# Optimization experiments

Measured on AMD Instinct MI355X. Metric: run time of the kernel, lower is better.

The kernel has to match this reference:

```python
import jax, jax.numpy as jnp
import numpy as np

H_SIZE = 128
E_SIZE = 16
N_LAYERS = 3
N_ATOMS = 80000
N_BLOCKS = 16000
N_EDGES = 320000
N_GRAPHS = 128


def setup_inputs() -> dict:
    key = jax.random.key(0)
    ks = jax.random.split(key, 20)
    p = lambda k, shape: (0.02 * jax.random.normal(k, shape, dtype=jnp.float32))
    h = H_SIZE
    inp = {
        'H': jax.random.normal(ks[0], (N_ATOMS, h), dtype=jnp.float32),
        'Z': jax.random.normal(ks[1], (N_ATOMS, 1, 3), dtype=jnp.float32),
        'block_id': jnp.sort(jax.random.randint(ks[2], (N_ATOMS,), 0, N_BLOCKS)),
        'batch_id': jnp.sort(jax.random.randint(ks[3], (N_BLOCKS,), 0, N_GRAPHS)),
        'edges': jax.random.randint(ks[4], (2, N_EDGES), 0, N_BLOCKS),
        'edge_attr': jax.random.normal(ks[5], (N_EDGES, E_SIZE), dtype=jnp.float32),
        # EGNN parameters
        'emb_in_w': p(ks[6], (h, h)), 'emb_in_b': jnp.zeros((h,), jnp.float32),
        'emb_out_w': p(ks[7], (h, h)), 'emb_out_b': jnp.zeros((h,), jnp.float32),
        'edge_w1': p(ks[8], (N_LAYERS, 2 * h + 1 + E_SIZE, h)), 'edge_b1': jnp.zeros((N_LAYERS, h), jnp.float32),
        'edge_w2': p(ks[9], (N_LAYERS, h, h)), 'edge_b2': jnp.zeros((N_LAYERS, h), jnp.float32),
        'node_w1': p(ks[10], (N_LAYERS, 2 * h, h)), 'node_b1': jnp.zeros((N_LAYERS, h), jnp.float32),
        'node_w2': p(ks[11], (N_LAYERS, h, h)), 'node_b2': jnp.zeros((N_LAYERS, h), jnp.float32),
        'coord_w1': p(ks[12], (N_LAYERS, h, h)), 'coord_b1': jnp.zeros((N_LAYERS, h), jnp.float32),
        'coord_w3': p(ks[13], (N_LAYERS, h, 1)),  # final coord layer, no bias
    }
    return inp


def _normalize(x, eps=1e-12):
    # F.normalize(dim=-1): x / max(||x||_2, eps)
    n = jnp.linalg.norm(x, axis=-1, keepdims=True)
    return x / jnp.maximum(n, eps)


def _seg_mean(x, ids, n):
    s = jax.ops.segment_sum(x, ids, num_segments=n)
    c = jax.ops.segment_sum(jnp.ones((x.shape[0], 1), x.dtype), ids, num_segments=n)
    return s / jnp.maximum(c, 1.0)


def _egnn_forward(H, Z, block_id, batch_id, edges, edge_attr,
                  emb_in_w, emb_in_b, emb_out_w, emb_out_b,
                  edge_w1, edge_b1, edge_w2, edge_b2,
                  node_w1, node_b1, node_w2, node_b2,
                  coord_w1, coord_b1, coord_w3):
    silu = jax.nn.silu
    # atom -> block pooling (scatter_mean)
    Hm = _seg_mean(H, block_id, N_BLOCKS)                      # [B, h]
    x = _seg_mean(Z.reshape(Z.shape[0], -1), block_id, N_BLOCKS)  # [B, 3] (squeeze of [B,1,3])
    row, col = edges[0], edges[1]

    h = Hm @ emb_in_w + emb_in_b
    for l in range(N_LAYERS):
        diff = x[row] - x[col]                                 # [E, 3]
        radial = jnp.sum(diff * diff, axis=-1, keepdims=True)  # [E, 1]
        e_in = jnp.concatenate([h[row], h[col], radial, edge_attr], axis=-1)  # [E, 2h+1+e]
        m = silu(silu(e_in @ edge_w1[l] + edge_b1[l]) @ edge_w2[l] + edge_b2[l])  # edge MLP [E, h]
        # coordinate update: per-edge scalar weight, mean aggregation
        w = silu(m @ coord_w1[l] + coord_b1[l]) @ coord_w3[l]  # [E, 1]
        x = x + _seg_mean(diff * w, row, N_BLOCKS)
        # node update: sum aggregation of messages, residual
        agg = jax.ops.segment_sum(m, row, num_segments=N_BLOCKS)  # [B, h]
        h = h + (silu(jnp.concatenate([h, agg], axis=-1) @ node_w1[l] + node_b1[l]) @ node_w2[l] + node_b2[l])
    h = h @ emb_out_w + emb_out_b

    block_repr = _normalize(h)                                  # [B, h]
    graph_repr = _normalize(jax.ops.segment_sum(block_repr, batch_id, num_segments=N_GRAPHS))  # [G, h]
    return Hm, block_repr, graph_repr


def reference(H, Z, block_id, batch_id, edges, edge_attr,
              emb_in_w, emb_in_b, emb_out_w, emb_out_b,
              edge_w1, edge_b1, edge_w2, edge_b2,
              node_w1, node_b1, node_w2, node_b2,
              coord_w1, coord_b1, coord_w3):
    return _egnn_forward(H, Z, block_id, batch_id, edges, edge_attr,
                         emb_in_w, emb_in_b, emb_out_w, emb_out_b,
                         edge_w1, edge_b1, edge_w2, edge_b2,
                         node_w1, node_b1, node_w2, node_b2,
                         coord_w1, coord_b1, coord_w3)
```

## Files before the change

### kernel.cpp

```cpp
#include <hip/hip_runtime.h>

#define N_ATOMS  80000
#define N_BLOCKS 16000
#define N_EDGES  320000
#define N_GRAPHS 128
#define HS       128

typedef unsigned short ushortT;
typedef __attribute__((ext_vector_type(8))) __bf16 bf16x8;
typedef __attribute__((ext_vector_type(8))) unsigned short ushort8;
typedef __attribute__((ext_vector_type(4))) float f32x4;

__device__ __forceinline__ unsigned short f2bf(float f){
  unsigned int u = __builtin_bit_cast(unsigned int, f);
  u = (u + 0x7FFFu + ((u >> 16) & 1u)) >> 16;
  return (unsigned short)u;
}
__device__ __forceinline__ ushortT f2bff(float f){
  __bf16 b = (__bf16)f;
  return __builtin_bit_cast(ushortT, b);
}
__device__ __forceinline__ float bf2f(ushortT u){
  unsigned int v = ((unsigned int)u) << 16;
  return __builtin_bit_cast(float, v);
}
__device__ __forceinline__ bf16x8 load8bf(const ushortT* p){
  uint4 u = *reinterpret_cast<const uint4*>(p);
  return __builtin_bit_cast(bf16x8, u);
}
__device__ __forceinline__ bf16x8 load8f_bf(const float* p){
  float4 a = *reinterpret_cast<const float4*>(p);
  float4 b = *reinterpret_cast<const float4*>(p + 4);
  ushort8 u = { f2bff(a.x), f2bff(a.y), f2bff(a.z), f2bff(a.w),
                f2bff(b.x), f2bff(b.y), f2bff(b.z), f2bff(b.w) };
  return __builtin_bit_cast(bf16x8, u);
}
__device__ __forceinline__ float silu(float v){
  return v * __builtin_amdgcn_rcpf(1.f + __expf(-v));
}

__device__ __forceinline__ int c_of_p(int p){
  int ks = p >> 5, lg = (p >> 3) & 3, j = p & 7;
  return 16 * (ks * 2 + (j >> 2)) + lg * 4 + (j & 3);
}

struct PrepParams {
  const float* ew1; const float* ew2; const float* cw1;
  const float* nw1; const float* nw2; const float* ei; const float* eo;
  const float* eb1;
  ushortT* W1atp; ushortT* W1btp; ushortT* W1ct; ushortT* W2tp; ushortT* CW1tp;
  ushortT* NW1t; ushortT* NW2t; ushortT* Eint; ushortT* Eoutt;
  float* b1p; int* hist;
};

__device__ __forceinline__ void tcvt(int idx, const float* __restrict__ src,
                                     ushortT* __restrict__ dst,
                                     int srcK, int row_off, int K, int N, int Kpad,
                                     int pn, int pk){
  int k = idx % Kpad;
  int rem = idx / Kpad;
  int n = rem % N;
  int l = rem / N;
  float v = 0.f;
  if (k < K){
    int kk = pk ? c_of_p(k) : k;
    int nn = pn ? c_of_p(n) : n;
    v = src[((size_t)l * srcK + row_off + kk) * N + nn];
  }
  dst[idx] = f2bf(v);
}

#define PREP_TOTAL (49152*5 + 12288 + 98304 + 16384*2 + 16000 + 384)

__global__ void prep_kernel(PrepParams P){
  int idx = blockIdx.x * 256 + threadIdx.x;
  if (idx < 49152){ tcvt(idx, P.ew1, P.W1atp, 273,   0, 128, 128, 128, 1, 0); return; }
  idx -= 49152;
  if (idx < 49152){ tcvt(idx, P.ew1, P.W1btp, 273, 128, 128, 128, 128, 1, 0); return; }
  idx -= 49152;
  if (idx < 12288){ tcvt(idx, P.ew1, P.W1ct,  273, 256,  17, 128,  32, 0, 0); return; }
  idx -= 12288;
  if (idx < 49152){ tcvt(idx, P.ew2, P.W2tp,  128,   0, 128, 128, 128, 0, 1); return; }
  idx -= 49152;
  if (idx < 49152){ tcvt(idx, P.cw1, P.CW1tp, 128,   0, 128, 128, 128, 0, 1); return; }
  idx -= 49152;
  if (idx < 98304){ tcvt(idx, P.nw1, P.NW1t,  256,   0, 256, 128, 256, 0, 0); return; }
  idx -= 98304;
  if (idx < 49152){ tcvt(idx, P.nw2, P.NW2t,  128,   0, 128, 128, 128, 0, 0); return; }
  idx -= 49152;
  if (idx < 16384){ tcvt(idx, P.ei,  P.Eint,  128,   0, 128, 128, 128, 0, 0); return; }
  idx -= 16384;
  if (idx < 16384){ tcvt(idx, P.eo,  P.Eoutt, 128,   0, 128, 128, 128, 0, 0); return; }
  idx -= 16384;
  if (idx < 16000){ P.hist[idx] = 0; return; }
  idx -= 16000;
  if (idx < 384){ int l = idx >> 7, p = idx & 127; P.b1p[idx] = P.eb1[l * 128 + c_of_p(p)]; }
}

__global__ void hist_bstart_kernel(const int* __restrict__ edges, int* __restrict__ hist,
                                   const int* __restrict__ bid, int* __restrict__ bstart){
  int b = blockIdx.x;
  if (b < N_EDGES / 256){
    int e = b * 256 + threadIdx.x;
    atomicAdd(&hist[edges[e]], 1);
  } else {
    int i = (b - N_EDGES / 256) * 256 + threadIdx.x;
    if (i <= N_BLOCKS){
      int lo = 0, hi = N_ATOMS;
      while (lo < hi){ int mid = (lo + hi) >> 1; if (bid[mid] < i) lo = mid + 1; else hi = mid; }
      bstart[i] = lo;
    }
  }
}

__global__ void scan_kernel(const int* __restrict__ hist, int* __restrict__ estart,
                            int* __restrict__ ecur){
  __shared__ int ps[256];
  int t = threadIdx.x;
  const int chunk = (N_BLOCKS + 255) / 256;
  int lo = t * chunk, hi = lo + chunk;
  if (hi > N_BLOCKS) hi = N_BLOCKS;
  int s = 0;
  for (int i = lo; i < hi; i++) s += hist[i];
  ps[t] = s;
  __syncthreads();
  for (int off = 1; off < 256; off <<= 1){
    int v = (t >= off) ? ps[t - off] : 0;
    __syncthreads();
    ps[t] += v;
    __syncthreads();
  }
  int base = (t == 0) ? 0 : ps[t - 1];
  for (int i = lo; i < hi; i++){ estart[i] = base; ecur[i] = base; base += hist[i]; }
  if (t == 255) estart[N_BLOCKS] = base;
}

__global__ void scatter_kernel(const int* __restrict__ edges, const float* __restrict__ attr,
                               int* __restrict__ ecur,
                               int* __restrict__ srow, int* __restrict__ scol,
                               ushortT* __restrict__ sattr){
  int e = blockIdx.x * 256 + threadIdx.x;
  if (e >= N_EDGES) return;
  int r = edges[e], c = edges[N_EDGES + e];
  int p = atomicAdd(&ecur[r], 1);
  srow[p] = r; scol[p] = c;
  ushortT buf[32];
  buf[0] = 0;
#pragma unroll
  for (int k = 0; k < 16; k++) buf[k + 1] = f2bf(attr[(size_t)e * 16 + k]);
#pragma unroll
  for (int k = 17; k < 32; k++) buf[k] = 0;
#pragma unroll
  for (int k = 0; k < 16; k++)
    reinterpret_cast<uint*>(sattr + (size_t)p * 32)[k] = reinterpret_cast<uint*>(buf)[k];
}

__global__ void pool_kernel(const float* __restrict__ H, const float* __restrict__ Z,
                            const int* __restrict__ start,
                            float* __restrict__ Hm, float* __restrict__ x,
                            float* __restrict__ gsum){
  int b = blockIdx.x;
  int t = threadIdx.x;
  if (b < 128) gsum[b * 128 + t] = 0.f;
  int s = start[b], e = start[b + 1];
  float inv = 1.f / (float)((e - s) > 0 ? (e - s) : 1);
  float sum = 0.f;
  for (int a = s; a < e; a++) sum += H[(size_t)a * HS + t];
  Hm[(size_t)b * HS + t] = sum * inv;
  if (t < 3){
    float sz = 0.f;
    for (int a = s; a < e; a++) sz += Z[a * 3 + t];
    x[b * 3 + t] = sz * inv;
  }
}

__global__ __launch_bounds__(256) void gemm_pq_kernel(
    const float* __restrict__ A,
    const ushortT* __restrict__ Wt, const float* __restrict__ bias,
    float* __restrict__ Cf,
    const ushortT* __restrict__ Wa, const ushortT* __restrict__ Wb,
    const float* __restrict__ b1p,
    ushortT* __restrict__ Pbf, ushortT* __restrict__ Qbf,
    float* __restrict__ agg, float* __restrict__ xacc){
  __shared__ __align__(16) ushortT t1_s[4][2048];
  int t = threadIdx.x; int lane = t & 63; int wv = t >> 6;
  int l15 = lane & 15, lg = lane >> 4;
  int base = blockIdx.x * 64 + wv * 16;
  int row = base + l15;
  {
    float4 z4 = {0.f, 0.f, 0.f, 0.f};
    float4* aggp = reinterpret_cast<float4*>(agg + (size_t)blockIdx.x * 64 * HS);
#pragma unroll
    for (int i = 0; i < 8; i++) aggp[t + 256 * i] = z4;
    if (t < 192) xacc[blockIdx.x * 192 + t] = 0.f;
  }
  ushortT* T1 = t1_s[wv];
  f32x4 zero = {0.f, 0.f, 0.f, 0.f};
  f32x4 acc[8];
#pragma unroll
  for (int n = 0; n < 8; n++) acc[n] = zero;
#pragma unroll
  for (int ks = 0; ks < 4; ks++){
    int k0 = ks * 32 + lg * 8;
    bf16x8 af = load8f_bf(A + (size_t)row * HS + k0);
#pragma unroll
    for (int n = 0; n < 8; n++){
      bf16x8 bf = load8bf(Wt + (size_t)(16 * n + l15) * HS + k0);
      acc[n] = __builtin_amdgcn_mfma_f32_16x16x32_bf16(af, bf, acc[n], 0, 0, 0);
    }
  }
#pragma unroll
  for (int n = 0; n < 8; n++){
    int col = 16 * n + l15;
    float bv = bias[col];
#pragma unroll
    for (int r = 0; r < 4; r++){
      int ro = base + lg * 4 + r;
      int er = lg * 4 + r;
      float hv = acc[n][r] + bv;
      Cf[(size_t)ro * HS + col] = hv;
      T1[(er * 128 + col) ^ ((er & 7) << 3)] = f2bff(hv);
    }
  }
  f32x4 accp[8], accq[8];
#pragma unroll
  for (int n = 0; n < 8; n++){ accp[n] = zero; accq[n] = zero; }
#pragma unroll
  for (int ks = 0; ks < 4; ks++){
    int k0 = ks * 32 + lg * 8;
    bf16x8 af = load8bf(&T1[(l15 * 128 + k0) ^ ((l15 & 7) << 3)]);
#pragma unroll
    for (int n = 0; n < 8; n++){
      accp[n] = __builtin_amdgcn_mfma_f32_16x16x32_bf16(af, load8bf(Wa + (size_t)(16 * n + l15) * HS + k0), accp[n], 0, 0, 0);
      accq[n] = __builtin_amdgcn_mfma_f32_16x16x32_bf16(af, load8bf(Wb + (size_t)(16 * n + l15) * HS + k0), accq[n], 0, 0, 0);
    }
  }
#pragma unroll
  for (int n = 0; n < 8; n++){
    int col = 16 * n + l15;
    float bv = b1p[col];
#pragma unroll
    for (int r = 0; r < 4; r++){
      int ro = base + lg * 4 + r;
      Pbf[(size_t)ro * HS + col] = f2bff(accp[n][r] + bv);
      Qbf[(size_t)ro * HS + col] = f2bff(accq[n][r]);
    }
  }
}

template<bool PQ>
__global__ __launch_bounds__(256) void node_kernel(
    float* __restrict__ h, float* __restrict__ agg,
    const ushortT* __restrict__ W1t, const ushortT* __restrict__ W2t,
    const float* __restrict__ b1, const float* __restrict__ b2,
    const ushortT* __restrict__ Wa, const ushortT* __restrict__ Wb,
    const float* __restrict__ b1p,
    ushortT* __restrict__ Pbf, ushortT* __restrict__ Qbf,
    float* __restrict__ x, float* __restrict__ xacc, const int* __restrict__ estart){
  __shared__ __align__(16) ushortT t1_s[4][2048];
  int t = threadIdx.x; int lane = t & 63; int wv = t >> 6;
  int l15 = lane & 15, lg = lane >> 4;
  int base = blockIdx.x * 64 + wv * 16;
  int row = base + l15;
  ushortT* T1 = t1_s[wv];
  f32x4 zero = {0.f, 0.f, 0.f, 0.f};

  if (PQ){
    if (t < 192){
      int i = blockIdx.x * 192 + t;
      int b = i / 3;
      int cnt = estart[b + 1] - estart[b];
      x[i] += xacc[i] / (float)(cnt > 0 ? cnt : 1);
      xacc[i] = 0.f;
    }
  }

  f32x4 acc[8];
#pragma unroll
  for (int n = 0; n < 8; n++) acc[n] = zero;
#pragma unroll
  for (int ks = 0; ks < 8; ks++){
    int k0 = ks * 32 + lg * 8;
    bf16x8 af = (k0 < 128) ? load8f_bf(h + (size_t)row * HS + k0)
                           : load8f_bf(agg + (size_t)row * HS + (k0 - 128));
#pragma unroll
    for (int n = 0; n < 8; n++){
      acc[n] = __builtin_amdgcn_mfma_f32_16x16x32_bf16(af, load8bf(W1t + (size_t)(16 * n + l15) * 256 + k0), acc[n], 0, 0, 0);
    }
  }
  if (PQ){
    __syncthreads();
    float4 z4 = {0.f, 0.f, 0.f, 0.f};
    float4* aggp = reinterpret_cast<float4*>(agg + (size_t)blockIdx.x * 64 * HS);
#pragma unroll
    for (int i = 0; i < 8; i++) aggp[t + 256 * i] = z4;
  }
#pragma unroll
  for (int n = 0; n < 8; n++){
    int col = 16 * n + l15;
    float bv = b1[col];
#pragma unroll
    for (int r = 0; r < 4; r++){
      int er = lg * 4 + r;
      T1[(er * 128 + col) ^ ((er & 7) << 3)] = f2bff(silu(acc[n][r] + bv));
    }
  }
#pragma unroll
  for (int n = 0; n < 8; n++) acc[n] = zero;
#pragma unroll
  for (int ks = 0; ks < 4; ks++){
    int k0 = ks * 32 + lg * 8;
    bf16x8 af = load8bf(&T1[(l15 * 128 + k0) ^ ((l15 & 7) << 3)]);
#pragma unroll
    for (int n = 0; n < 8; n++){
      acc[n] = __builtin_amdgcn_mfma_f32_16x16x32_bf16(af, load8bf(W2t + (size_t)(16 * n + l15) * HS + k0), acc[n], 0, 0, 0);
    }
  }
#pragma unroll
  for (int n = 0; n < 8; n++){
    int col = 16 * n + l15;
    float bv = b2[col];
#pragma unroll
    for (int r = 0; r < 4; r++){
      int ro = base + lg * 4 + r;
      int er = lg * 4 + r;
      float hv = h[(size_t)ro * HS + col] + acc[n][r] + bv;
      h[(size_t)ro * HS + col] = hv;
      if (PQ) T1[(er * 128 + col) ^ ((er & 7) << 3)] = f2bff(hv);
    }
  }
  if (PQ){
    f32x4 accp[8], accq[8];
#pragma unroll
    for (int n = 0; n < 8; n++){ accp[n] = zero; accq[n] = zero; }
#pragma unroll
    for (int ks = 0; ks < 4; ks++){
      int k0 = ks * 32 + lg * 8;
      bf16x8 af = load8bf(&T1[(l15 * 128 + k0) ^ ((l15 & 7) << 3)]);
#pragma unroll
      for (int n = 0; n < 8; n++){
        accp[n] = __builtin_amdgcn_mfma_f32_16x16x32_bf16(af, load8bf(Wa + (size_t)(16 * n + l15) * HS + k0), accp[n], 0, 0, 0);
        accq[n] = __builtin_amdgcn_mfma_f32_16x16x32_bf16(af, load8bf(Wb + (size_t)(16 * n + l15) * HS + k0), accq[n], 0, 0, 0);
      }
    }
#pragma unroll
    for (int n = 0; n < 8; n++){
      int col = 16 * n + l15;
      float bv = b1p[col];
#pragma unroll
      for (int r = 0; r < 4; r++){
        int ro = base + lg * 4 + r;
        Pbf[(size_t)ro * HS + col] = f2bff(accp[n][r] + bv);
        Qbf[(size_t)ro * HS + col] = f2bff(accq[n][r]);
      }
    }
  }
}

__global__ __launch_bounds__(256) void emb_norm_kernel(
    const float* __restrict__ h, const ushortT* __restrict__ Wt,
    const float* __restrict__ bias, const int* __restrict__ batch_id,
    float* __restrict__ brep, float* __restrict__ gsum){
  int t = threadIdx.x; int lane = t & 63; int wv = t >> 6;
  int l15 = lane & 15, lg = lane >> 4;
  int base = blockIdx.x * 64 + wv * 16;
  int row = base + l15;
  f32x4 zero = {0.f, 0.f, 0.f, 0.f};
  f32x4 acc[8];
#pragma unroll
  for (int n = 0; n < 8; n++) acc[n] = zero;
#pragma unroll
  for (int ks = 0; ks < 4; ks++){
    int k0 = ks * 32 + lg * 8;
    bf16x8 af = load8f_bf(h + (size_t)row * HS + k0);
#pragma unroll
    for (int n = 0; n < 8; n++){
      acc[n] = __builtin_amdgcn_mfma_f32_16x16x32_bf16(af, load8bf(Wt + (size_t)(16 * n + l15) * HS + k0), acc[n], 0, 0, 0);
    }
  }
#pragma unroll
  for (int n = 0; n < 8; n++){
    float bv = bias[16 * n + l15];
#pragma unroll
    for (int r = 0; r < 4; r++) acc[n][r] += bv;
  }
  float scl[4];
#pragma unroll
  for (int r = 0; r < 4; r++){
    float ss = 0.f;
#pragma unroll
    for (int n = 0; n < 8; n++) ss += acc[n][r] * acc[n][r];
#pragma unroll
    for (int o = 1; o < 16; o <<= 1) ss += __shfl_xor(ss, o, 64);
    scl[r] = 1.f / fmaxf(sqrtf(ss), 1e-12f);
  }
#pragma unroll
  for (int r = 0; r < 4; r++){
    int ro = base + lg * 4 + r;
    int g = batch_id[ro];
#pragma unroll
    for (int n = 0; n < 8; n++){
      int col = 16 * n + l15;
      float v = acc[n][r] * scl[r];
      brep[(size_t)ro * HS + col] = v;
      atomicAdd(&gsum[g * HS + col], v);
    }
  }
}

template<int COORD>
__global__ __launch_bounds__(256, 4) void edge_kernel(
    const int* __restrict__ srow, const int* __restrict__ scol,
    const ushortT* __restrict__ sattr,
    const float* __restrict__ x,
    const ushortT* __restrict__ Pbf, const ushortT* __restrict__ Qbf,
    const ushortT* __restrict__ W1ct, const ushortT* __restrict__ W2tp,
    const ushortT* __restrict__ CW1tp,
    const float* __restrict__ b2, const float* __restrict__ cb1,
    const float* __restrict__ cw3,
    float* __restrict__ xacc, float* __restrict__ agg){
  __shared__ float bias_l[3][128];
  __shared__ int   rid_s[64];
  __shared__ float dif_s[COORD ? 64 : 1][3];
  __shared__ float wall[COORD ? 4 : 1][COORD ? 64 : 1];
  __shared__ __align__(16) ushortT S1[64 * 128];
  __shared__ __align__(16) ushortT S2[64 * 128];

  const int t = threadIdx.x;
  const int lane = t & 63;
  const int wv = t >> 6;
  const int l15 = lane & 15, lg = lane >> 4;
  const f32x4 zero = {0.f, 0.f, 0.f, 0.f};

  if (t < 128){
    bias_l[0][t] = b2[t];
    if (COORD){ bias_l[1][t] = cb1[t]; bias_l[2][t] = cw3[t]; }
  }

  const int erow = wv * 16 + l15;
  const int e = blockIdx.x * 64 + erow;
  const int r = srow[e], c = scol[e];
  const float dx = x[r * 3 + 0] - x[c * 3 + 0];
  const float dy = x[r * 3 + 1] - x[c * 3 + 1];
  const float dz = x[r * 3 + 2] - x[c * 3 + 2];
  const float rad = dx * dx + dy * dy + dz * dz;
  if (lg == 0){
    rid_s[erow] = r;
    if (COORD){ dif_s[erow][0] = dx; dif_s[erow][1] = dy; dif_s[erow][2] = dz; }
  }
  ushort8 at8 = __builtin_bit_cast(ushort8, load8bf(sattr + (size_t)e * 32 + lg * 8));
  if (lg == 0) at8[0] = f2bff(rad);
  const bf16x8 atb = __builtin_bit_cast(bf16x8, at8);

#pragma unroll
  for (int ks = 0; ks < 4; ks++){
    f32x4 a0 = __builtin_amdgcn_mfma_f32_16x16x32_bf16(
        load8bf(W1ct + (size_t)(16 * (2 * ks)     + l15) * 32 + lg * 8), atb, zero, 0, 0, 0);
    f32x4 a1 = __builtin_amdgcn_mfma_f32_16x16x32_bf16(
        load8bf(W1ct + (size_t)(16 * (2 * ks + 1) + l15) * 32 + lg * 8), atb, zero, 0, 0, 0);
    ushort8 pv = __builtin_bit_cast(ushort8, load8bf(Pbf + (size_t)r * HS + ks * 32 + lg * 8));
    ushort8 qv = __builtin_bit_cast(ushort8, load8bf(Qbf + (size_t)c * HS + ks * 32 + lg * 8));
    ushort8 af;
#pragma unroll
    for (int j = 0; j < 4; j++)
      af[j] = f2bff(silu(a0[j] + bf2f(pv[j]) + bf2f(qv[j])));
#pragma unroll
    for (int j = 4; j < 8; j++)
      af[j] = f2bff(silu(a1[j - 4] + bf2f(pv[j]) + bf2f(qv[j])));
    int byte = (erow * 256 + ks * 64 + lg * 16) ^ ((erow & 7) << 4);
    *reinterpret_cast<uint4*>(reinterpret_cast<char*>(S1) + byte) = __builtin_bit_cast(uint4, af);
  }
  __syncthreads();

  f32x4 acc2[4][2];
#pragma unroll
  for (int et = 0; et < 4; et++){ acc2[et][0] = zero; acc2[et][1] = zero; }
#pragma unroll
  for (int ks = 0; ks < 4; ks++){
    bf16x8 wf0 = load8bf(W2tp + (size_t)(16 * (2 * wv)     + l15) * HS + ks * 32 + lg * 8);
    bf16x8 wf1 = load8bf(W2tp + (size_t)(16 * (2 * wv + 1) + l15) * HS + ks * 32 + lg * 8);
#pragma unroll
    for (int et = 0; et < 4; et++){
      int row2 = et * 16 + l15;
      int byte = (row2 * 256 + ks * 64 + lg * 16) ^ ((row2 & 7) << 4);
      bf16x8 mb = __builtin_bit_cast(bf16x8,
          *reinterpret_cast<const uint4*>(reinterpret_cast<const char*>(S1) + byte));
      acc2[et][0] = __builtin_amdgcn_mfma_f32_16x16x32_bf16(wf0, mb, acc2[et][0], 0, 0, 0);
      acc2[et][1] = __builtin_amdgcn_mfma_f32_16x16x32_bf16(wf1, mb, acc2[et][1], 0, 0, 0);
    }
  }
#pragma unroll
  for (int g = 0; g < 2; g++){
    int n = 2 * wv + g;
    float4 bv = *reinterpret_cast<const float4*>(&bias_l[0][16 * n + lg * 4]);
    int pbyte = ((n >> 1) * 32 + lg * 8 + (n & 1) * 4) * 2;
#pragma unroll
    for (int et = 0; et < 4; et++){
      ushortT mm[4];
#pragma unroll
      for (int rr = 0; rr < 4; rr++)
        mm[rr] = f2bff(silu(acc2[et][g][rr] + (&bv.x)[rr]));
      int row2 = et * 16 + l15;
      int byte = (row2 * 256 + pbyte) ^ ((row2 & 7) << 4);
      *reinterpret_cast<uint2*>(reinterpret_cast<char*>(S2) + byte) =
          *reinterpret_cast<uint2*>(mm);
    }
  }
  __syncthreads();

  if (COORD){
    f32x4 acc3[4][2];
#pragma unroll
    for (int et = 0; et < 4; et++){ acc3[et][0] = zero; acc3[et][1] = zero; }
#pragma unroll
    for (int ks = 0; ks < 4; ks++){
      bf16x8 wf0 = load8bf(CW1tp + (size_t)(16 * (2 * wv)     + l15) * HS + ks * 32 + lg * 8);
      bf16x8 wf1 = load8bf(CW1tp + (size_t)(16 * (2 * wv + 1) + l15) * HS + ks * 32 + lg * 8);
#pragma unroll
      for (int et = 0; et < 4; et++){
        int row2 = et * 16 + l15;
        int byte = (row2 * 256 + ks * 64 + lg * 16) ^ ((row2 & 7) << 4);
        bf16x8 mb = __builtin_bit_cast(bf16x8,
            *reinterpret_cast<const uint4*>(reinterpret_cast<const char*>(S2) + byte));
        acc3[et][0] = __builtin_amdgcn_mfma_f32_16x16x32_bf16(wf0, mb, acc3[et][0], 0, 0, 0);
        acc3[et][1] = __builtin_amdgcn_mfma_f32_16x16x32_bf16(wf1, mb, acc3[et][1], 0, 0, 0);
      }
    }
#pragma unroll
    for (int et = 0; et < 4; et++){
      float ws = 0.f;
#pragma unroll
      for (int g = 0; g < 2; g++){
        int n = 2 * wv + g;
        float4 cbv = *reinterpret_cast<const float4*>(&bias_l[1][16 * n + lg * 4]);
        float4 cwv = *reinterpret_cast<const float4*>(&bias_l[2][16 * n + lg * 4]);
#pragma unroll
        for (int rr = 0; rr < 4; rr++)
          ws += silu(acc3[et][g][rr] + (&cbv.x)[rr]) * (&cwv.x)[rr];
      }
      ws += __shfl_xor(ws, 16, 64);
      ws += __shfl_xor(ws, 32, 64);
      if (lg == 0) wall[wv][et * 16 + l15] = ws;
    }
  }

  {
    const int c0 = c_of_p(2 * lane), c1 = c_of_p(2 * lane + 1);
    float run0 = 0.f, run1 = 0.f;
    int prev = __builtin_amdgcn_readfirstlane(rid_s[wv * 16]);
#pragma unroll
    for (int e2 = 0; e2 < 16; e2++){
      int re = __builtin_amdgcn_readfirstlane(rid_s[wv * 16 + e2]);
      if (re != prev){
        atomicAdd(&agg[(size_t)prev * HS + c0], run0);
        atomicAdd(&agg[(size_t)prev * HS + c1], run1);
        run0 = 0.f; run1 = 0.f; prev = re;
      }
      int row2 = wv * 16 + e2;
      int byte = (row2 * 256 + lane * 4) ^ ((row2 & 7) << 4);
      uint u = *reinterpret_cast<const uint*>(reinterpret_cast<const char*>(S2) + byte);
      run0 += bf2f((ushortT)(u & 0xFFFF));
      run1 += bf2f((ushortT)(u >> 16));
    }
    atomicAdd(&agg[(size_t)prev * HS + c0], run0);
    atomicAdd(&agg[(size_t)prev * HS + c1], run1);
  }

  if (COORD){
    __syncthreads();
    if (t < 192){
      int e2 = t / 3, cd = t % 3;
      float w = wall[0][e2] + wall[1][e2] + wall[2][e2] + wall[3][e2];
      atomicAdd(&xacc[(size_t)rid_s[e2] * 3 + cd], dif_s[e2][cd] * w);
    }
  }
}

__global__ void norm_graph_kernel(const float* __restrict__ gsum, float* __restrict__ grep){
  int wv = threadIdx.x >> 6, lane = threadIdx.x & 63;
  int g = blockIdx.x * 4 + wv;
  if (g >= N_GRAPHS) return;
  float v0 = gsum[g * HS + lane];
  float v1 = gsum[g * HS + 64 + lane];
  float ss = v0 * v0 + v1 * v1;
#pragma unroll
  for (int o = 1; o < 64; o <<= 1) ss += __shfl_xor(ss, o, 64);
  float s = 1.f / fmaxf(sqrtf(ss), 1e-12f);
  grep[(size_t)g * HS + lane] = v0 * s;
  grep[(size_t)g * HS + 64 + lane] = v1 * s;
}

extern "C" void kernel_launch(void* const* d_in, const int* in_sizes, int n_in,
                              void* d_out, int out_size, void* d_ws, size_t ws_size,
                              hipStream_t stream){
  const float* H         = (const float*)d_in[0];
  const float* Z         = (const float*)d_in[1];
  const int*   block_id  = (const int*)d_in[2];
  const int*   batch_id  = (const int*)d_in[3];
  const int*   edges     = (const int*)d_in[4];
  const float* edge_attr = (const float*)d_in[5];
  const float* emb_in_w  = (const float*)d_in[6];
  const float* emb_in_b  = (const float*)d_in[7];
  const float* emb_out_w = (const float*)d_in[8];
  const float* emb_out_b = (const float*)d_in[9];
  const float* edge_w1   = (const float*)d_in[10];
  const float* edge_b1   = (const float*)d_in[11];
  const float* edge_w2   = (const float*)d_in[12];
  const float* edge_b2   = (const float*)d_in[13];
  const float* node_w1   = (const float*)d_in[14];
  const float* node_b1   = (const float*)d_in[15];
  const float* node_w2   = (const float*)d_in[16];
  const float* node_b2   = (const float*)d_in[17];
  const float* coord_w1  = (const float*)d_in[18];
  const float* coord_b1  = (const float*)d_in[19];
  const float* coord_w3  = (const float*)d_in[20];

  float* out  = (float*)d_out;
  float* Hm   = out;
  float* brep = out + (size_t)N_BLOCKS * HS;
  float* grep = out + (size_t)2 * N_BLOCKS * HS;

  char* base = (char*)d_ws;
  size_t off = 0;
  auto take = [&](size_t bytes) -> char* {
    char* p = base + off;
    off += (bytes + 255) & ~(size_t)255;
    return p;
  };
  float*   x     = (float*)  take((size_t)N_BLOCKS * 3 * 4);
  float*   xacc  = (float*)  take((size_t)N_BLOCKS * 3 * 4);
  float*   h     = (float*)  take((size_t)N_BLOCKS * HS * 4);
  float*   agg   = (float*)  take((size_t)N_BLOCKS * HS * 4);
  float*   gsum  = (float*)  take((size_t)N_GRAPHS * HS * 4);
  int*     bstart= (int*)    take((size_t)(N_BLOCKS + 1) * 4);
  int*     hist  = (int*)    take((size_t)N_BLOCKS * 4);
  int*     estart= (int*)    take((size_t)(N_BLOCKS + 1) * 4);
  int*     ecur  = (int*)    take((size_t)N_BLOCKS * 4);
  int*     srow  = (int*)    take((size_t)N_EDGES * 4);
  int*     scol  = (int*)    take((size_t)N_EDGES * 4);
  ushortT* sattr = (ushortT*)take((size_t)N_EDGES * 32 * 2);
  ushortT* Pbf   = (ushortT*)take((size_t)N_BLOCKS * HS * 2);
  ushortT* Qbf   = (ushortT*)take((size_t)N_BLOCKS * HS * 2);
  ushortT* W1atp = (ushortT*)take((size_t)3 * 128 * 128 * 2);
  ushortT* W1btp = (ushortT*)take((size_t)3 * 128 * 128 * 2);
  ushortT* W1ct  = (ushortT*)take((size_t)3 * 128 * 32 * 2);
  ushortT* W2tp  = (ushortT*)take((size_t)3 * 128 * 128 * 2);
  ushortT* CW1tp = (ushortT*)take((size_t)3 * 128 * 128 * 2);
  ushortT* NW1t  = (ushortT*)take((size_t)3 * 128 * 256 * 2);
  ushortT* NW2t  = (ushortT*)take((size_t)3 * 128 * 128 * 2);
  ushortT* Eint  = (ushortT*)take((size_t)128 * 128 * 2);
  ushortT* Eoutt = (ushortT*)take((size_t)128 * 128 * 2);
  float*   b1p   = (float*)  take((size_t)3 * 128 * 4);

  PrepParams P;
  P.ew1 = edge_w1; P.ew2 = edge_w2; P.cw1 = coord_w1;
  P.nw1 = node_w1; P.nw2 = node_w2; P.ei = emb_in_w; P.eo = emb_out_w;
  P.eb1 = edge_b1;
  P.W1atp = W1atp; P.W1btp = W1btp; P.W1ct = W1ct; P.W2tp = W2tp; P.CW1tp = CW1tp;
  P.NW1t = NW1t; P.NW2t = NW2t; P.Eint = Eint; P.Eoutt = Eoutt;
  P.b1p = b1p; P.hist = hist;
  prep_kernel<<<(PREP_TOTAL + 255) / 256, 256, 0, stream>>>(P);

  hist_bstart_kernel<<<N_EDGES / 256 + (N_BLOCKS + 1 + 255) / 256, 256, 0, stream>>>(
      edges, hist, block_id, bstart);
  scan_kernel<<<1, 256, 0, stream>>>(hist, estart, ecur);
  scatter_kernel<<<N_EDGES / 256, 256, 0, stream>>>(edges, edge_attr, ecur, srow, scol, sattr);
  pool_kernel<<<N_BLOCKS, 128, 0, stream>>>(H, Z, bstart, Hm, x, gsum);

  gemm_pq_kernel<<<N_BLOCKS / 64, 256, 0, stream>>>(Hm, Eint, emb_in_b, h,
                                                    W1atp, W1btp, b1p, Pbf, Qbf, agg, xacc);

  for (int l = 0; l < 3; l++){
    if (l < 2){
      edge_kernel<1><<<N_EDGES / 64, 256, 0, stream>>>(
          srow, scol, sattr, x, Pbf, Qbf,
          W1ct + (size_t)l * 128 * 32, W2tp + (size_t)l * 128 * 128, CW1tp + (size_t)l * 128 * 128,
          edge_b2 + l * 128, coord_b1 + l * 128, coord_w3 + l * 128,
          xacc, agg);
      node_kernel<true><<<N_BLOCKS / 64, 256, 0, stream>>>(
          h, agg, NW1t + (size_t)l * 128 * 256, NW2t + (size_t)l * 128 * 128,
          node_b1 + l * 128, node_b2 + l * 128,
          W1atp + (size_t)(l + 1) * 128 * 128, W1btp + (size_t)(l + 1) * 128 * 128,
          b1p + (l + 1) * 128, Pbf, Qbf, x, xacc, estart);
    } else {
      edge_kernel<0><<<N_EDGES / 64, 256, 0, stream>>>(
          srow, scol, sattr, x, Pbf, Qbf,
          W1ct + (size_t)l * 128 * 32, W2tp + (size_t)l * 128 * 128, CW1tp + (size_t)l * 128 * 128,
          edge_b2 + l * 128, coord_b1 + l * 128, coord_w3 + l * 128,
          xacc, agg);
      node_kernel<false><<<N_BLOCKS / 64, 256, 0, stream>>>(
          h, agg, NW1t + (size_t)l * 128 * 256, NW2t + (size_t)l * 128 * 128,
          node_b1 + l * 128, node_b2 + l * 128,
          nullptr, nullptr, nullptr, nullptr, nullptr, nullptr, nullptr, nullptr);
    }
  }

  emb_norm_kernel<<<N_BLOCKS / 64, 256, 0, stream>>>(h, Eoutt, emb_out_b, batch_id, brep, gsum);
  norm_graph_kernel<<<N_GRAPHS / 4, 256, 0, stream>>>(gsum, grep);
}
```

Before: 531.9 us.

## Fuse final node update with output embedding, shrink node blocks, widen scan

Merges the last-layer node update with the output embedding and normalisation into one kernel, so h does not make an extra global round-trip and one launch is dropped. The node and gemm kernels move from four-wave blocks of 64 rows to single-wave blocks of 16 rows, giving more blocks for better load spread. The scan now uses 1024 threads. In the edge kernel each wave keeps its own message slice in registers rather than reading it back from shared memory. More blocks could add scheduling overhead, and fewer waves per block may hide latency less well.

```diff
diff --git a/kernel.cpp b/kernel.cpp
--- a/kernel.cpp
+++ b/kernel.cpp
@@ -113,18 +113,20 @@
   }
 }
 
-__global__ void scan_kernel(const int* __restrict__ hist, int* __restrict__ estart,
-                            int* __restrict__ ecur){
-  __shared__ int ps[256];
+__global__ __launch_bounds__(1024) void scan_kernel(const int* __restrict__ hist,
+                                                    int* __restrict__ estart,
+                                                    int* __restrict__ ecur){
+  __shared__ int ps[1024];
   int t = threadIdx.x;
-  const int chunk = (N_BLOCKS + 255) / 256;
+  const int chunk = (N_BLOCKS + 1023) / 1024;
   int lo = t * chunk, hi = lo + chunk;
   if (hi > N_BLOCKS) hi = N_BLOCKS;
+  if (lo > N_BLOCKS) lo = N_BLOCKS;
   int s = 0;
   for (int i = lo; i < hi; i++) s += hist[i];
   ps[t] = s;
   __syncthreads();
-  for (int off = 1; off < 256; off <<= 1){
+  for (int off = 1; off < 1024; off <<= 1){
     int v = (t >= off) ? ps[t - off] : 0;
     __syncthreads();
     ps[t] += v;
@@ -132,7 +134,7 @@
   }
   int base = (t == 0) ? 0 : ps[t - 1];
   for (int i = lo; i < hi; i++){ estart[i] = base; ecur[i] = base; base += hist[i]; }
-  if (t == 255) estart[N_BLOCKS] = base;
+  if (t == 1023) estart[N_BLOCKS] = base;
 }
 
 __global__ void scatter_kernel(const int* __restrict__ edges, const float* __restrict__ attr,
@@ -174,7 +176,7 @@
   }
 }
 
-__global__ __launch_bounds__(256) void gemm_pq_kernel(
+__global__ __launch_bounds__(64) void gemm_pq_kernel(
     const float* __restrict__ A,
     const ushortT* __restrict__ Wt, const float* __restrict__ bias,
     float* __restrict__ Cf,
@@ -182,19 +184,18 @@
     const float* __restrict__ b1p,
     ushortT* __restrict__ Pbf, ushortT* __restrict__ Qbf,
     float* __restrict__ agg, float* __restrict__ xacc){
-  __shared__ __align__(16) ushortT t1_s[4][2048];
-  int t = threadIdx.x; int lane = t & 63; int wv = t >> 6;
+  __shared__ __align__(16) ushortT T1[2048];
+  int lane = threadIdx.x;
   int l15 = lane & 15, lg = lane >> 4;
-  int base = blockIdx.x * 64 + wv * 16;
+  int base = blockIdx.x * 16;
   int row = base + l15;
   {
     float4 z4 = {0.f, 0.f, 0.f, 0.f};
-    float4* aggp = reinterpret_cast<float4*>(agg + (size_t)blockIdx.x * 64 * HS);
-#pragma unroll
-    for (int i = 0; i < 8; i++) aggp[t + 256 * i] = z4;
-    if (t < 192) xacc[blockIdx.x * 192 + t] = 0.f;
-  }
-  ushortT* T1 = t1_s[wv];
+    float4* aggp = reinterpret_cast<float4*>(agg + (size_t)blockIdx.x * 16 * HS);
+#pragma unroll
+    for (int i = 0; i < 8; i++) aggp[lane + 64 * i] = z4;
+    if (lane < 48) xacc[blockIdx.x * 48 + lane] = 0.f;
+  }
   f32x4 zero = {0.f, 0.f, 0.f, 0.f};
   f32x4 acc[8];
 #pragma unroll
@@ -248,8 +249,7 @@
   }
 }
 
-template<bool PQ>
-__global__ __launch_bounds__(256) void node_kernel(
+__global__ __launch_bounds__(64) void node_pq_kernel(
     float* __restrict__ h, float* __restrict__ agg,
     const ushortT* __restrict__ W1t, const ushortT* __restrict__ W2t,
     const float* __restrict__ b1, const float* __restrict__ b2,
@@ -257,22 +257,19 @@
     const float* __restrict__ b1p,
     ushortT* __restrict__ Pbf, ushortT* __restrict__ Qbf,
     float* __restrict__ x, float* __restrict__ xacc, const int* __restrict__ estart){
-  __shared__ __align__(16) ushortT t1_s[4][2048];
-  int t = threadIdx.x; int lane = t & 63; int wv = t >> 6;
+  __shared__ __align__(16) ushortT T1[2048];
+  int lane = threadIdx.x;
   int l15 = lane & 15, lg = lane >> 4;
-  int base = blockIdx.x * 64 + wv * 16;
+  int base = blockIdx.x * 16;
   int row = base + l15;
-  ushortT* T1 = t1_s[wv];
   f32x4 zero = {0.f, 0.f, 0.f, 0.f};
 
-  if (PQ){
-    if (t < 192){
-      int i = blockIdx.x * 192 + t;
-      int b = i / 3;
-      int cnt = estart[b + 1] - estart[b];
-      x[i] += xacc[i] / (float)(cnt > 0 ? cnt : 1);
-      xacc[i] = 0.f;
-    }
+  if (lane < 48){
+    int i = blockIdx.x * 48 + lane;
+    int b = i / 3;
+    int cnt = estart[b + 1] - estart[b];
+    x[i] += xacc[i] / (float)(cnt > 0 ? cnt : 1);
+    xacc[i] = 0.f;
   }
 
   f32x4 acc[8];
@@ -288,12 +285,12 @@
       acc[n] = __builtin_amdgcn_mfma_f32_16x16x32_bf16(af, load8bf(W1t + (size_t)(16 * n + l15) * 256 + k0), acc[n], 0, 0, 0);
     }
   }
-  if (PQ){
-    __syncthreads();
+  __syncthreads();
+  {
     float4 z4 = {0.f, 0.f, 0.f, 0.f};
-    float4* aggp = reinterpret_cast<float4*>(agg + (size_t)blockIdx.x * 64 * HS);
-#pragma unroll
-    for (int i = 0; i < 8; i++) aggp[t + 256 * i] = z4;
+    float4* aggp = reinterpret_cast<float4*>(agg + (size_t)blockIdx.x * 16 * HS);
+#pragma unroll
+    for (int i = 0; i < 8; i++) aggp[lane + 64 * i] = z4;
   }
 #pragma unroll
   for (int n = 0; n < 8; n++){
@@ -326,61 +323,109 @@
       int er = lg * 4 + r;
       float hv = h[(size_t)ro * HS + col] + acc[n][r] + bv;
       h[(size_t)ro * HS + col] = hv;
-      if (PQ) T1[(er * 128 + col) ^ ((er & 7) << 3)] = f2bff(hv);
-    }
-  }
-  if (PQ){
-    f32x4 accp[8], accq[8];
-#pragma unroll
-    for (int n = 0; n < 8; n++){ accp[n] = zero; accq[n] = zero; }
-#pragma unroll
-    for (int ks = 0; ks < 4; ks++){
-      int k0 = ks * 32 + lg * 8;
-      bf16x8 af = load8bf(&T1[(l15 * 128 + k0) ^ ((l15 & 7) << 3)]);
-#pragma unroll
-      for (int n = 0; n < 8; n++){
-        accp[n] = __builtin_amdgcn_mfma_f32_16x16x32_bf16(af, load8bf(Wa + (size_t)(16 * n + l15) * HS + k0), accp[n], 0, 0, 0);
-        accq[n] = __builtin_amdgcn_mfma_f32_16x16x32_bf16(af, load8bf(Wb + (size_t)(16 * n + l15) * HS + k0), accq[n], 0, 0, 0);
-      }
-    }
-#pragma unroll
-    for (int n = 0; n < 8; n++){
-      int col = 16 * n + l15;
-      float bv = b1p[col];
-#pragma unroll
-      for (int r = 0; r < 4; r++){
-        int ro = base + lg * 4 + r;
-        Pbf[(size_t)ro * HS + col] = f2bff(accp[n][r] + bv);
-        Qbf[(size_t)ro * HS + col] = f2bff(accq[n][r]);
-      }
-    }
-  }
-}
-
-__global__ __launch_bounds__(256) void emb_norm_kernel(
-    const float* __restrict__ h, const ushortT* __restrict__ Wt,
-    const float* __restrict__ bias, const int* __restrict__ batch_id,
+      T1[(er * 128 + col) ^ ((er & 7) << 3)] = f2bff(hv);
+    }
+  }
+  f32x4 accp[8], accq[8];
+#pragma unroll
+  for (int n = 0; n < 8; n++){ accp[n] = zero; accq[n] = zero; }
+#pragma unroll
+  for (int ks = 0; ks < 4; ks++){
+    int k0 = ks * 32 + lg * 8;
+    bf16x8 af = load8bf(&T1[(l15 * 128 + k0) ^ ((l15 & 7) << 3)]);
+#pragma unroll
+    for (int n = 0; n < 8; n++){
+      accp[n] = __builtin_amdgcn_mfma_f32_16x16x32_bf16(af, load8bf(Wa + (size_t)(16 * n + l15) * HS + k0), accp[n], 0, 0, 0);
+      accq[n] = __builtin_amdgcn_mfma_f32_16x16x32_bf16(af, load8bf(Wb + (size_t)(16 * n + l15) * HS + k0), accq[n], 0, 0, 0);
+    }
+  }
+#pragma unroll
+  for (int n = 0; n < 8; n++){
+    int col = 16 * n + l15;
+    float bv = b1p[col];
+#pragma unroll
+    for (int r = 0; r < 4; r++){
+      int ro = base + lg * 4 + r;
+      Pbf[(size_t)ro * HS + col] = f2bff(accp[n][r] + bv);
+      Qbf[(size_t)ro * HS + col] = f2bff(accq[n][r]);
+    }
+  }
+}
+
+__global__ __launch_bounds__(64) void node_emb_kernel(
+    const float* __restrict__ h, const float* __restrict__ agg,
+    const ushortT* __restrict__ W1t, const ushortT* __restrict__ W2t,
+    const float* __restrict__ b1, const float* __restrict__ b2,
+    const ushortT* __restrict__ Eoutt, const float* __restrict__ eob,
+    const int* __restrict__ batch_id,
     float* __restrict__ brep, float* __restrict__ gsum){
-  int t = threadIdx.x; int lane = t & 63; int wv = t >> 6;
+  __shared__ __align__(16) ushortT T1[2048];
+  int lane = threadIdx.x;
   int l15 = lane & 15, lg = lane >> 4;
-  int base = blockIdx.x * 64 + wv * 16;
+  int base = blockIdx.x * 16;
   int row = base + l15;
   f32x4 zero = {0.f, 0.f, 0.f, 0.f};
+
   f32x4 acc[8];
+#pragma unroll
+  for (int n = 0; n < 8; n++) acc[n] = zero;
+#pragma unroll
+  for (int ks = 0; ks < 8; ks++){
+    int k0 = ks * 32 + lg * 8;
+    bf16x8 af = (k0 < 128) ? load8f_bf(h + (size_t)row * HS + k0)
+                           : load8f_bf(agg + (size_t)row * HS + (k0 - 128));
+#pragma unroll
+    for (int n = 0; n < 8; n++){
+      acc[n] = __builtin_amdgcn_mfma_f32_16x16x32_bf16(af, load8bf(W1t + (size_t)(16 * n + l15) * 256 + k0), acc[n], 0, 0, 0);
+    }
+  }
+#pragma unroll
+  for (int n = 0; n < 8; n++){
+    int col = 16 * n + l15;
+    float bv = b1[col];
+#pragma unroll
+    for (int r = 0; r < 4; r++){
+      int er = lg * 4 + r;
+      T1[(er * 128 + col) ^ ((er & 7) << 3)] = f2bff(silu(acc[n][r] + bv));
+    }
+  }
 #pragma unroll
   for (int n = 0; n < 8; n++) acc[n] = zero;
 #pragma unroll
   for (int ks = 0; ks < 4; ks++){
     int k0 = ks * 32 + lg * 8;
-    bf16x8 af = load8f_bf(h + (size_t)row * HS + k0);
-#pragma unroll
-    for (int n = 0; n < 8; n++){
-      acc[n] = __builtin_amdgcn_mfma_f32_16x16x32_bf16(af, load8bf(Wt + (size_t)(16 * n + l15) * HS + k0), acc[n], 0, 0, 0);
+    bf16x8 af = load8bf(&T1[(l15 * 128 + k0) ^ ((l15 & 7) << 3)]);
+#pragma unroll
+    for (int n = 0; n < 8; n++){
+      acc[n] = __builtin_amdgcn_mfma_f32_16x16x32_bf16(af, load8bf(W2t + (size_t)(16 * n + l15) * HS + k0), acc[n], 0, 0, 0);
     }
   }
 #pragma unroll
   for (int n = 0; n < 8; n++){
-    float bv = bias[16 * n + l15];
+    int col = 16 * n + l15;
+    float bv = b2[col];
+#pragma unroll
+    for (int r = 0; r < 4; r++){
+      int ro = base + lg * 4 + r;
+      int er = lg * 4 + r;
+      float hv = h[(size_t)ro * HS + col] + acc[n][r] + bv;
+      T1[(er * 128 + col) ^ ((er & 7) << 3)] = f2bff(hv);
+    }
+  }
+#pragma unroll
+  for (int n = 0; n < 8; n++) acc[n] = zero;
+#pragma unroll
+  for (int ks = 0; ks < 4; ks++){
+    int k0 = ks * 32 + lg * 8;
+    bf16x8 af = load8bf(&T1[(l15 * 128 + k0) ^ ((l15 & 7) << 3)]);
+#pragma unroll
+    for (int n = 0; n < 8; n++){
+      acc[n] = __builtin_amdgcn_mfma_f32_16x16x32_bf16(af, load8bf(Eoutt + (size_t)(16 * n + l15) * HS + k0), acc[n], 0, 0, 0);
+    }
+  }
+#pragma unroll
+  for (int n = 0; n < 8; n++){
+    float bv = eob[16 * n + l15];
 #pragma unroll
     for (int r = 0; r < 4; r++) acc[n][r] += bv;
   }
@@ -489,22 +534,21 @@
       acc2[et][1] = __builtin_amdgcn_mfma_f32_16x16x32_bf16(wf1, mb, acc2[et][1], 0, 0, 0);
     }
   }
-#pragma unroll
-  for (int g = 0; g < 2; g++){
-    int n = 2 * wv + g;
-    float4 bv = *reinterpret_cast<const float4*>(&bias_l[0][16 * n + lg * 4]);
-    int pbyte = ((n >> 1) * 32 + lg * 8 + (n & 1) * 4) * 2;
-#pragma unroll
-    for (int et = 0; et < 4; et++){
-      ushortT mm[4];
+  ushort8 mreg[4];
+#pragma unroll
+  for (int et = 0; et < 4; et++){
+    ushort8 mq;
+#pragma unroll
+    for (int g = 0; g < 2; g++){
+      float4 bv = *reinterpret_cast<const float4*>(&bias_l[0][16 * (2 * wv + g) + lg * 4]);
 #pragma unroll
       for (int rr = 0; rr < 4; rr++)
-        mm[rr] = f2bff(silu(acc2[et][g][rr] + (&bv.x)[rr]));
-      int row2 = et * 16 + l15;
-      int byte = (row2 * 256 + pbyte) ^ ((row2 & 7) << 4);
-      *reinterpret_cast<uint2*>(reinterpret_cast<char*>(S2) + byte) =
-          *reinterpret_cast<uint2*>(mm);
-    }
+        mq[g * 4 + rr] = f2bff(silu(acc2[et][g][rr] + (&bv.x)[rr]));
+    }
+    mreg[et] = mq;
+    int row2 = et * 16 + l15;
+    int byte = (row2 * 256 + wv * 64 + lg * 16) ^ ((row2 & 7) << 4);
+    *reinterpret_cast<uint4*>(reinterpret_cast<char*>(S2) + byte) = __builtin_bit_cast(uint4, mq);
   }
   __syncthreads();
 
@@ -518,10 +562,15 @@
       bf16x8 wf1 = load8bf(CW1tp + (size_t)(16 * (2 * wv + 1) + l15) * HS + ks * 32 + lg * 8);
 #pragma unroll
       for (int et = 0; et < 4; et++){
-        int row2 = et * 16 + l15;
-        int byte = (row2 * 256 + ks * 64 + lg * 16) ^ ((row2 & 7) << 4);
-        bf16x8 mb = __builtin_bit_cast(bf16x8,
-            *reinterpret_cast<const uint4*>(reinterpret_cast<const char*>(S2) + byte));
+        bf16x8 mb;
+        if (ks == wv){
+          mb = __builtin_bit_cast(bf16x8, mreg[et]);
+        } else {
+          int row2 = et * 16 + l15;
+          int byte = (row2 * 256 + ks * 64 + lg * 16) ^ ((row2 & 7) << 4);
+          mb = __builtin_bit_cast(bf16x8,
+              *reinterpret_cast<const uint4*>(reinterpret_cast<const char*>(S2) + byte));
+        }
         acc3[et][0] = __builtin_amdgcn_mfma_f32_16x16x32_bf16(wf0, mb, acc3[et][0], 0, 0, 0);
         acc3[et][1] = __builtin_amdgcn_mfma_f32_16x16x32_bf16(wf1, mb, acc3[et][1], 0, 0, 0);
       }
@@ -663,12 +712,12 @@
 
   hist_bstart_kernel<<<N_EDGES / 256 + (N_BLOCKS + 1 + 255) / 256, 256, 0, stream>>>(
       edges, hist, block_id, bstart);
-  scan_kernel<<<1, 256, 0, stream>>>(hist, estart, ecur);
+  scan_kernel<<<1, 1024, 0, stream>>>(hist, estart, ecur);
   scatter_kernel<<<N_EDGES / 256, 256, 0, stream>>>(edges, edge_attr, ecur, srow, scol, sattr);
   pool_kernel<<<N_BLOCKS, 128, 0, stream>>>(H, Z, bstart, Hm, x, gsum);
 
-  gemm_pq_kernel<<<N_BLOCKS / 64, 256, 0, stream>>>(Hm, Eint, emb_in_b, h,
-                                                    W1atp, W1btp, b1p, Pbf, Qbf, agg, xacc);
+  gemm_pq_kernel<<<N_BLOCKS / 16, 64, 0, stream>>>(Hm, Eint, emb_in_b, h,
+                                                   W1atp, W1btp, b1p, Pbf, Qbf, agg, xacc);
 
   for (int l = 0; l < 3; l++){
     if (l < 2){
@@ -677,7 +726,7 @@
           W1ct + (size_t)l * 128 * 32, W2tp + (size_t)l * 128 * 128, CW1tp + (size_t)l * 128 * 128,
           edge_b2 + l * 128, coord_b1 + l * 128, coord_w3 + l * 128,
           xacc, agg);
-      node_kernel<true><<<N_BLOCKS / 64, 256, 0, stream>>>(
+      node_pq_kernel<<<N_BLOCKS / 16, 64, 0, stream>>>(
           h, agg, NW1t + (size_t)l * 128 * 256, NW2t + (size_t)l * 128 * 128,
           node_b1 + l * 128, node_b2 + l * 128,
           W1atp + (size_t)(l + 1) * 128 * 128, W1btp + (size_t)(l + 1) * 128 * 128,
@@ -688,13 +737,12 @@
           W1ct + (size_t)l * 128 * 32, W2tp + (size_t)l * 128 * 128, CW1tp + (size_t)l * 128 * 128,
           edge_b2 + l * 128, coord_b1 + l * 128, coord_w3 + l * 128,
           xacc, agg);
-      node_kernel<false><<<N_BLOCKS / 64, 256, 0, stream>>>(
+      node_emb_kernel<<<N_BLOCKS / 16, 64, 0, stream>>>(
           h, agg, NW1t + (size_t)l * 128 * 256, NW2t + (size_t)l * 128 * 128,
           node_b1 + l * 128, node_b2 + l * 128,
-          nullptr, nullptr, nullptr, nullptr, nullptr, nullptr, nullptr, nullptr);
-    }
-  }
-
-  emb_norm_kernel<<<N_BLOCKS / 64, 256, 0, stream>>>(h, Eoutt, emb_out_b, batch_id, brep, gsum);
+          Eoutt, emb_out_b, batch_id, brep, gsum);
+    }
+  }
+
   norm_graph_kernel<<<N_GRAPHS / 4, 256, 0, stream>>>(gsum, grep);
 }
```

After: 521.5 us (median of 2 runs). Within noise of the previous version (-2.0%).
